# Kernel optimization log

Measured on AMD Instinct MI355X. Metric: run time of the kernel, lower is better.

## Reference

```python
import jax, jax.numpy as jnp
import numpy as np


def _gcn_layer(ann, adj, Wa, ba, W2, b2):
    # ann: [B,N,F], adj: [B,E,N,N], Wa: [E,F,U], ba: [E,U], W2: [F,U], b2: [U]
    # per-edge-type linear, fused as one batched einsum -> [B,E,N,U]
    h = jnp.einsum('bnf,efu->benu', ann, Wa) + ba[None, :, None, :]
    # adjacency matmul per edge type: [B,E,N,N] @ [B,E,N,U]
    h = jnp.einsum('benm,bemu->benu', adj, h)
    # sum over edge types + residual linear + activation (tanh)
    out = h.sum(axis=1) + jnp.einsum('bnf,fu->bnu', ann, W2) + b2
    return jnp.tanh(out)


def setup_inputs() -> dict:
    key = jax.random.key(0)
    ks = jax.random.split(key, 10)
    B, N, F, E, U = 32, 1024, 32, 4, 32
    s = 1.0 / np.sqrt(F)
    s1 = 1.0 / np.sqrt(F + U)
    return {
        'n_tensor': jax.random.normal(ks[0], (B, N, F), dtype=jnp.float32),
        'adj_tensor': jax.random.uniform(ks[1], (B, E, N, N), dtype=jnp.float32),
        'W_adj0': jax.random.normal(ks[2], (E, F, U), dtype=jnp.float32) * s,
        'b_adj0': jax.random.normal(ks[3], (E, U), dtype=jnp.float32) * s,
        'W2_0': jax.random.normal(ks[4], (F, U), dtype=jnp.float32) * s,
        'b2_0': jax.random.normal(ks[5], (U,), dtype=jnp.float32) * s,
        'W_adj1': jax.random.normal(ks[6], (E, F + U, U), dtype=jnp.float32) * s1,
        'b_adj1': jax.random.normal(ks[7], (E, U), dtype=jnp.float32) * s1,
        'W2_1': jax.random.normal(ks[8], (F + U, U), dtype=jnp.float32) * s1,
        'b2_1': jax.random.normal(ks[9], (U,), dtype=jnp.float32) * s1,
    }


def reference(n_tensor, adj_tensor, W_adj0, b_adj0, W2_0, b2_0,
              W_adj1, b_adj1, W2_1, b2_1):
    # layer 0: h_tensor is None -> annotations = n_tensor
    h = _gcn_layer(n_tensor, adj_tensor, W_adj0, b_adj0, W2_0, b2_0)
    # layer 1: annotations = cat(n_tensor, hidden)
    ann1 = jnp.concatenate([n_tensor, h], axis=-1)
    h = _gcn_layer(ann1, adj_tensor, W_adj1, b_adj1, W2_1, b2_1)
    return h
```

## Files before the change

kernel.cpp:

```cpp
#include <hip/hip_runtime.h>
#include <math.h>

#define Bb 32
#define Nn 1024
#define Ee 4
#define Uu 32

template <int F, int FA>
__global__ __launch_bounds__(256) void pre_kernel(
    const float* __restrict__ annA, const float* __restrict__ annB,
    const float* __restrict__ Wa, const float* __restrict__ ba,
    const float* __restrict__ W2, const float* __restrict__ b2,
    float* __restrict__ hpre_t, float* __restrict__ res)
{
    const int e = blockIdx.y;
    __shared__ float wlds[F * Uu];
    __shared__ float blds[Uu];
    const int tid = threadIdx.x;
    const float* wsrc = (e < 4) ? (Wa + (size_t)e * F * Uu) : W2;
    const float* bsrc = (e < 4) ? (ba + (size_t)e * Uu) : b2;
    for (int i = tid; i < F * Uu; i += 256) wlds[i] = wsrc[i];
    if (tid < Uu) blds[tid] = bsrc[tid];
    __syncthreads();

    const int g = blockIdx.x * 256 + tid;
    const int b = g >> 10;
    const int n = g & 1023;

    float4 a4[F / 4];
    {
        const float4* rA = (const float4*)(annA + (size_t)g * FA);
#pragma unroll
        for (int i = 0; i < FA / 4; ++i) a4[i] = rA[i];
        if constexpr (F > FA) {
            const float4* rB = (const float4*)(annB + (size_t)g * (F - FA));
#pragma unroll
            for (int i = 0; i < (F - FA) / 4; ++i) a4[FA / 4 + i] = rB[i];
        }
    }

    float4 acc[8];
    const float4* bb = (const float4*)blds;
#pragma unroll
    for (int uq = 0; uq < 8; ++uq) acc[uq] = bb[uq];
    const float4* w4 = (const float4*)wlds;
#pragma unroll
    for (int f4 = 0; f4 < F / 4; ++f4) {
        const float4 av = a4[f4];
#pragma unroll
        for (int c = 0; c < 4; ++c) {
            const float s = (c == 0) ? av.x : (c == 1) ? av.y : (c == 2) ? av.z : av.w;
#pragma unroll
            for (int uq = 0; uq < 8; ++uq) {
                const float4 w = w4[(f4 * 4 + c) * 8 + uq];
                acc[uq].x = fmaf(s, w.x, acc[uq].x);
                acc[uq].y = fmaf(s, w.y, acc[uq].y);
                acc[uq].z = fmaf(s, w.z, acc[uq].z);
                acc[uq].w = fmaf(s, w.w, acc[uq].w);
            }
        }
    }
    if (e < 4) {
        float* dst = hpre_t + ((size_t)(b * 4 + e) * Uu) * Nn + n;
#pragma unroll
        for (int uq = 0; uq < 8; ++uq) {
            dst[(uq * 4 + 0) * Nn] = acc[uq].x;
            dst[(uq * 4 + 1) * Nn] = acc[uq].y;
            dst[(uq * 4 + 2) * Nn] = acc[uq].z;
            dst[(uq * 4 + 3) * Nn] = acc[uq].w;
        }
    } else {
        float4* dst = (float4*)(res + (size_t)g * Uu);
#pragma unroll
        for (int uq = 0; uq < 8; ++uq) dst[uq] = acc[uq];
    }
}

__global__ __launch_bounds__(256) void gcn_main_kernel(
    const float* __restrict__ adj,
    const float* __restrict__ hpre_t,
    const float* __restrict__ res,
    float* __restrict__ out)
{
    __shared__ float hbuf[2][Uu * 64];

    const int bid = blockIdx.x;
    const int swz = (bid & 7) * 128 + (bid >> 3);
    const int b = swz >> 5;
    const int n0 = (swz & 31) * 32;
    const int tid = threadIdx.x;
    const int w = tid >> 6;
    const int lane = tid & 63;
    const int gu = lane >> 4;
    const int ms = lane & 15;
    const int wrow = n0 + w * 8;

    float acc[8][8];
#pragma unroll
    for (int r = 0; r < 8; ++r)
#pragma unroll
        for (int j = 0; j < 8; ++j) acc[r][j] = 0.f;

    const float* adjb = adj + (size_t)b * Ee * Nn * Nn;
    const float* hpb = hpre_t + (size_t)b * Ee * Uu * Nn;

    const int fi0 = tid, fi1 = tid + 256;
    const int su0 = fi0 >> 4, sm0 = fi0 & 15;
    const int su1 = fi1 >> 4, sm1 = fi1 & 15;

    float4 adjA[8], adjB[8];
    float4 h0, h1;

    {
        const float* ap = adjb + (size_t)wrow * Nn + ms * 4;
#pragma unroll
        for (int r = 0; r < 8; ++r) adjA[r] = *(const float4*)(ap + (size_t)r * Nn);
        h0 = *(const float4*)(hpb + (size_t)su0 * Nn + sm0 * 4);
        h1 = *(const float4*)(hpb + (size_t)su1 * Nn + sm1 * 4);
    }

#define GCN_BODY(CUR, ALT, T)                                                   \
    {                                                                           \
        const int t_ = (T);                                                     \
        float* hb = hbuf[t_ & 1];                                               \
        ((float4*)hb)[fi0] = h0;                  \
        ((float4*)hb)[fi1] = h1;                                                \
        const int tn_ = (t_ < 63) ? t_ + 1 : 63;                                \
        const int e2_ = tn_ >> 4, c2_ = tn_ & 15;                               \
        const float* ap_ = adjb + ((size_t)e2_ * Nn + wrow) * Nn + c2_ * 64 + ms * 4; \
        _Pragma("unroll")                                                       \
        for (int r = 0; r < 8; ++r) ALT[r] = *(const float4*)(ap_ + (size_t)r * Nn); \
        const float* hc_ = hpb + (size_t)e2_ * Uu * Nn + c2_ * 64;              \
        h0 = *(const float4*)(hc_ + (size_t)su0 * Nn + sm0 * 4);                \
        h1 = *(const float4*)(hc_ + (size_t)su1 * Nn + sm1 * 4);                \
        asm volatile("s_waitcnt lgkmcnt(0)" ::: "memory");                      \
        __builtin_amdgcn_s_barrier();                                           \
        __builtin_amdgcn_sched_barrier(0);                                      \
        _Pragma("unroll")                                                       \
        for (int j = 0; j < 8; ++j) {                                           \
            const float4 hv = *(const float4*)(hb + (gu * 8 + j) * 64 + ms * 4); \
            _Pragma("unroll")                                                   \
            for (int r = 0; r < 8; ++r) {                                       \
                float t = fmaf(CUR[r].x, hv.x, acc[r][j]);                      \
                t = fmaf(CUR[r].y, hv.y, t);                                    \
                t = fmaf(CUR[r].z, hv.z, t);                                    \
                acc[r][j] = fmaf(CUR[r].w, hv.w, t);                            \
            }                                                                   \
        }                                                                       \
    }

    for (int t = 0; t < 64; t += 2) {
        GCN_BODY(adjA, adjB, t);
        GCN_BODY(adjB, adjA, t + 1);
    }
#undef GCN_BODY

#pragma unroll
    for (int r = 0; r < 8; ++r)
#pragma unroll
        for (int j = 0; j < 8; ++j) {
            float v = acc[r][j];
            v += __shfl_xor(v, 1);
            v += __shfl_xor(v, 2);
            v += __shfl_xor(v, 4);
            v += __shfl_xor(v, 8);
            acc[r][j] = v;
        }

#pragma unroll
    for (int r = 0; r < 8; ++r) {
        if (ms == r) {
            const int n = wrow + r;
            const float* rp = res + ((size_t)b * Nn + n) * Uu + gu * 8;
            float* op = out + ((size_t)b * Nn + n) * Uu + gu * 8;
            const float4 r0 = *(const float4*)(rp);
            const float4 r1 = *(const float4*)(rp + 4);
            float4 o0, o1;
            o0.x = tanhf(acc[r][0] + r0.x);
            o0.y = tanhf(acc[r][1] + r0.y);
            o0.z = tanhf(acc[r][2] + r0.z);
            o0.w = tanhf(acc[r][3] + r0.w);
            o1.x = tanhf(acc[r][4] + r1.x);
            o1.y = tanhf(acc[r][5] + r1.y);
            o1.z = tanhf(acc[r][6] + r1.z);
            o1.w = tanhf(acc[r][7] + r1.w);
            *(float4*)(op) = o0;
            *(float4*)(op + 4) = o1;
        }
    }
}

extern "C" void kernel_launch(void* const* d_in, const int* in_sizes, int n_in,
                              void* d_out, int out_size, void* d_ws, size_t ws_size,
                              hipStream_t stream)
{
    const float* n_tensor = (const float*)d_in[0];
    const float* adj      = (const float*)d_in[1];
    const float* W_adj0   = (const float*)d_in[2];
    const float* b_adj0   = (const float*)d_in[3];
    const float* W2_0     = (const float*)d_in[4];
    const float* b2_0     = (const float*)d_in[5];
    const float* W_adj1   = (const float*)d_in[6];
    const float* b_adj1   = (const float*)d_in[7];
    const float* W2_1     = (const float*)d_in[8];
    const float* b2_1     = (const float*)d_in[9];
    float* outp = (float*)d_out;

    float* ws   = (float*)d_ws;
    float* hpre = ws;
    float* resb = ws + (size_t)4 * 1024 * 1024;
    float* h0   = ws + (size_t)5 * 1024 * 1024;

    dim3 pre_grid(128, 5);

    pre_kernel<32, 32><<<pre_grid, 256, 0, stream>>>(n_tensor, nullptr, W_adj0, b_adj0,
                                                     W2_0, b2_0, hpre, resb);
    gcn_main_kernel<<<1024, 256, 0, stream>>>(adj, hpre, resb, h0);

    pre_kernel<64, 32><<<pre_grid, 256, 0, stream>>>(n_tensor, h0, W_adj1, b_adj1,
                                                     W2_1, b2_1, hpre, resb);
    gcn_main_kernel<<<1024, 256, 0, stream>>>(adj, hpre, resb, outp);
}
```

Before: 426.9 us.

## Triple-buffer GCN main loop with direct global-to-LDS loads and smaller row tiles

Rewrites the adjacency-matmul main loop as a three-stage pipeline. The hidden-feature tiles are loaded straight into LDS with global_load_lds instead of being staged through registers, and the loop waits on vmcnt before a barrier. Each block now covers 16 rows instead of 32, launched over 2048 blocks, with 4 rows per wave, which halves the accumulator and adjacency register footprint and allows more waves in flight for this memory-bound stream of adj reads. The cost is twice as many loads of the hidden tile per batch, plus reliance on hand-counted vmcnt values for correctness.

```diff
diff --git a/kernel.cpp b/kernel.cpp
--- a/kernel.cpp
+++ b/kernel.cpp
@@ -1,7 +1,6 @@
 #include <hip/hip_runtime.h>
 #include <math.h>
 
-#define Bb 32
 #define Nn 1024
 #define Ee 4
 #define Uu 32
@@ -82,81 +81,90 @@
     const float* __restrict__ res,
     float* __restrict__ out)
 {
-    __shared__ float hbuf[2][Uu * 64];
+    __shared__ float hbuf[3][Uu * 64];
 
     const int bid = blockIdx.x;
-    const int swz = (bid & 7) * 128 + (bid >> 3);
-    const int b = swz >> 5;
-    const int n0 = (swz & 31) * 32;
+    const int swz = (bid & 7) * 256 + (bid >> 3);
+    const int b = swz >> 6;
+    const int n0 = (swz & 63) * 16;
     const int tid = threadIdx.x;
     const int w = tid >> 6;
     const int lane = tid & 63;
     const int gu = lane >> 4;
     const int ms = lane & 15;
-    const int wrow = n0 + w * 8;
-
-    float acc[8][8];
-#pragma unroll
-    for (int r = 0; r < 8; ++r)
+    const int wrow = n0 + w * 4;
+
+    const float* adjb = adj + (size_t)b * Ee * Nn * Nn;
+    const float* hpb  = hpre_t + (size_t)b * Ee * Uu * Nn;
+    const int l4 = lane >> 4, l15 = lane & 15;
+
+    float acc[4][8];
+#pragma unroll
+    for (int r = 0; r < 4; ++r)
 #pragma unroll
         for (int j = 0; j < 8; ++j) acc[r][j] = 0.f;
 
-    const float* adjb = adj + (size_t)b * Ee * Nn * Nn;
-    const float* hpb = hpre_t + (size_t)b * Ee * Uu * Nn;
-
-    const int fi0 = tid, fi1 = tid + 256;
-    const int su0 = fi0 >> 4, sm0 = fi0 & 15;
-    const int su1 = fi1 >> 4, sm1 = fi1 & 15;
-
-    float4 adjA[8], adjB[8];
-    float4 h0, h1;
-
-    {
-        const float* ap = adjb + (size_t)wrow * Nn + ms * 4;
-#pragma unroll
-        for (int r = 0; r < 8; ++r) adjA[r] = *(const float4*)(ap + (size_t)r * Nn);
-        h0 = *(const float4*)(hpb + (size_t)su0 * Nn + sm0 * 4);
-        h1 = *(const float4*)(hpb + (size_t)su1 * Nn + sm1 * 4);
-    }
-
-#define GCN_BODY(CUR, ALT, T)                                                   \
+    float4 av0[4], av1[4], av2[4];
+
+#define ISSUE(AV, PH, T)                                                        \
     {                                                                           \
-        const int t_ = (T);                                                     \
-        float* hb = hbuf[t_ & 1];                                               \
-        ((float4*)hb)[fi0] = h0;                  \
-        ((float4*)hb)[fi1] = h1;                                                \
-        const int tn_ = (t_ < 63) ? t_ + 1 : 63;                                \
-        const int e2_ = tn_ >> 4, c2_ = tn_ & 15;                               \
-        const float* ap_ = adjb + ((size_t)e2_ * Nn + wrow) * Nn + c2_ * 64 + ms * 4; \
+        const int e_ = (T) >> 4, c_ = (T) & 15;                                 \
+        const float* ap_ = adjb + ((size_t)(e_ * Nn + wrow)) * Nn + c_ * 64 + ms * 4; \
+        AV[0] = *(const float4*)(ap_);                                          \
+        AV[1] = *(const float4*)(ap_ + Nn);                                     \
+        AV[2] = *(const float4*)(ap_ + 2 * Nn);                                 \
+        AV[3] = *(const float4*)(ap_ + 3 * Nn);                                 \
+        const float* hs_ = hpb + (size_t)e_ * Uu * Nn + c_ * 64 + l15 * 4;      \
+        __builtin_amdgcn_global_load_lds(                                       \
+            (const __attribute__((address_space(1))) void*)(hs_ + (size_t)(8 * w + l4) * Nn),     \
+            (__attribute__((address_space(3))) void*)(&hbuf[PH][(8 * w) * 64]), 16, 0, 0);        \
+        __builtin_amdgcn_global_load_lds(                                       \
+            (const __attribute__((address_space(1))) void*)(hs_ + (size_t)(8 * w + 4 + l4) * Nn), \
+            (__attribute__((address_space(3))) void*)(&hbuf[PH][(8 * w + 4) * 64]), 16, 0, 0);    \
+    }
+
+#define COMPUTE(AV, PH)                                                         \
+    {                                                                           \
         _Pragma("unroll")                                                       \
-        for (int r = 0; r < 8; ++r) ALT[r] = *(const float4*)(ap_ + (size_t)r * Nn); \
-        const float* hc_ = hpb + (size_t)e2_ * Uu * Nn + c2_ * 64;              \
-        h0 = *(const float4*)(hc_ + (size_t)su0 * Nn + sm0 * 4);                \
-        h1 = *(const float4*)(hc_ + (size_t)su1 * Nn + sm1 * 4);                \
-        asm volatile("s_waitcnt lgkmcnt(0)" ::: "memory");                      \
+        for (int j = 0; j < 8; ++j) {                                           \
+            const float4 hv = *(const float4*)(&hbuf[PH][(gu * 8 + j) * 64 + ms * 4]); \
+            _Pragma("unroll")                                                   \
+            for (int r = 0; r < 4; ++r) {                                       \
+                float t0 = fmaf(AV[r].x, hv.x, acc[r][j]);                      \
+                t0 = fmaf(AV[r].y, hv.y, t0);                                   \
+                t0 = fmaf(AV[r].z, hv.z, t0);                                   \
+                acc[r][j] = fmaf(AV[r].w, hv.w, t0);                            \
+            }                                                                   \
+        }                                                                       \
+    }
+
+#define WAITBAR(N)                                                              \
+    {                                                                           \
+        __builtin_amdgcn_sched_barrier(0);                                      \
+        asm volatile("s_waitcnt vmcnt(" #N ")" ::: "memory");                   \
         __builtin_amdgcn_s_barrier();                                           \
         __builtin_amdgcn_sched_barrier(0);                                      \
-        _Pragma("unroll")                                                       \
-        for (int j = 0; j < 8; ++j) {                                           \
-            const float4 hv = *(const float4*)(hb + (gu * 8 + j) * 64 + ms * 4); \
-            _Pragma("unroll")                                                   \
-            for (int r = 0; r < 8; ++r) {                                       \
-                float t = fmaf(CUR[r].x, hv.x, acc[r][j]);                      \
-                t = fmaf(CUR[r].y, hv.y, t);                                    \
-                t = fmaf(CUR[r].z, hv.z, t);                                    \
-                acc[r][j] = fmaf(CUR[r].w, hv.w, t);                            \
-            }                                                                   \
-        }                                                                       \
-    }
-
-    for (int t = 0; t < 64; t += 2) {
-        GCN_BODY(adjA, adjB, t);
-        GCN_BODY(adjB, adjA, t + 1);
-    }
-#undef GCN_BODY
-
-#pragma unroll
-    for (int r = 0; r < 8; ++r)
+    }
+
+    ISSUE(av0, 0, 0);
+    ISSUE(av1, 1, 1);
+
+    for (int t = 0; t < 60; t += 3) {
+        WAITBAR(6); ISSUE(av2, 2, t + 2); COMPUTE(av0, 0);
+        WAITBAR(6); ISSUE(av0, 0, t + 3); COMPUTE(av1, 1);
+        WAITBAR(6); ISSUE(av1, 1, t + 4); COMPUTE(av2, 2);
+    }
+    WAITBAR(6); ISSUE(av2, 2, 62); COMPUTE(av0, 0);
+    WAITBAR(6); ISSUE(av0, 0, 63); COMPUTE(av1, 1);
+    WAITBAR(6); COMPUTE(av2, 2);
+    WAITBAR(0); COMPUTE(av0, 0);
+
+#undef ISSUE
+#undef COMPUTE
+#undef WAITBAR
+
+#pragma unroll
+    for (int r = 0; r < 4; ++r)
 #pragma unroll
         for (int j = 0; j < 8; ++j) {
             float v = acc[r][j];
@@ -168,7 +176,7 @@
         }
 
 #pragma unroll
-    for (int r = 0; r < 8; ++r) {
+    for (int r = 0; r < 4; ++r) {
         if (ms == r) {
             const int n = wrow + r;
             const float* rp = res + ((size_t)b * Nn + n) * Uu + gu * 8;
@@ -215,9 +223,9 @@
 
     pre_kernel<32, 32><<<pre_grid, 256, 0, stream>>>(n_tensor, nullptr, W_adj0, b_adj0,
                                                      W2_0, b2_0, hpre, resb);
-    gcn_main_kernel<<<1024, 256, 0, stream>>>(adj, hpre, resb, h0);
+    gcn_main_kernel<<<2048, 256, 0, stream>>>(adj, hpre, resb, h0);
 
     pre_kernel<64, 32><<<pre_grid, 256, 0, stream>>>(n_tensor, h0, W_adj1, b_adj1,
                                                      W2_1, b2_1, hpre, resb);
-    gcn_main_kernel<<<1024, 256, 0, stream>>>(adj, hpre, resb, outp);
+    gcn_main_kernel<<<2048, 256, 0, stream>>>(adj, hpre, resb, outp);
 }
```

Result: slower. 647.4 us (+51.6%).

## Split-K gcn main kernel across waves with direct h loads and LDS reduction

Applied to the files above, without the earlier changes.

Each block now covers 8 rows instead of 32, and the four waves split the m dimension (256 columns each) instead of splitting rows. Each wave loads the h tile directly from global memory into registers, which removes the LDS staging, the per-step barriers and the double-buffer pipeline. Partial sums from the four waves are combined through shared memory before the tanh epilogue. The grid grows fourfold for more parallelism, but h is now reloaded per wave from global/L2 and there is no explicit prefetch, so latency hiding depends on occupancy (launch_bounds 256,2).

```diff
diff --git a/kernel.cpp b/kernel.cpp
--- a/kernel.cpp
+++ b/kernel.cpp
@@ -1,7 +1,6 @@
 #include <hip/hip_runtime.h>
 #include <math.h>
 
-#define Bb 32
 #define Nn 1024
 #define Ee 4
 #define Uu 32
@@ -76,24 +75,27 @@
     }
 }
 
-__global__ __launch_bounds__(256) void gcn_main_kernel(
+__global__ __launch_bounds__(256, 2) void gcn_main_kernel(
     const float* __restrict__ adj,
     const float* __restrict__ hpre_t,
     const float* __restrict__ res,
     float* __restrict__ out)
 {
-    __shared__ float hbuf[2][Uu * 64];
+    __shared__ float part[4][8][Uu];
 
     const int bid = blockIdx.x;
-    const int swz = (bid & 7) * 128 + (bid >> 3);
-    const int b = swz >> 5;
-    const int n0 = (swz & 31) * 32;
+    const int swz = (bid & 7) * 512 + (bid >> 3);
+    const int b = swz >> 7;
+    const int n0 = (swz & 127) * 8;
     const int tid = threadIdx.x;
     const int w = tid >> 6;
     const int lane = tid & 63;
     const int gu = lane >> 4;
     const int ms = lane & 15;
-    const int wrow = n0 + w * 8;
+
+    const float* adjb = adj + (size_t)b * Ee * Nn * Nn;
+    const float* hpb  = hpre_t + (size_t)b * Ee * Uu * Nn;
+    const int mbase = w * 256 + ms * 4;
 
     float acc[8][8];
 #pragma unroll
@@ -101,59 +103,26 @@
 #pragma unroll
         for (int j = 0; j < 8; ++j) acc[r][j] = 0.f;
 
-    const float* adjb = adj + (size_t)b * Ee * Nn * Nn;
-    const float* hpb = hpre_t + (size_t)b * Ee * Uu * Nn;
-
-    const int fi0 = tid, fi1 = tid + 256;
-    const int su0 = fi0 >> 4, sm0 = fi0 & 15;
-    const int su1 = fi1 >> 4, sm1 = fi1 & 15;
-
-    float4 adjA[8], adjB[8];
-    float4 h0, h1;
-
-    {
-        const float* ap = adjb + (size_t)wrow * Nn + ms * 4;
+#pragma unroll 2
+    for (int it = 0; it < 16; ++it) {
+        const int e = it >> 2, sub = it & 3;
+        const float* ap = adjb + ((size_t)e * Nn + n0) * Nn + mbase + sub * 64;
+        const float* hp = hpb + ((size_t)e * Uu + gu * 8) * Nn + mbase + sub * 64;
+        float4 av[8], hv[8];
 #pragma unroll
-        for (int r = 0; r < 8; ++r) adjA[r] = *(const float4*)(ap + (size_t)r * Nn);
-        h0 = *(const float4*)(hpb + (size_t)su0 * Nn + sm0 * 4);
-        h1 = *(const float4*)(hpb + (size_t)su1 * Nn + sm1 * 4);
+        for (int r = 0; r < 8; ++r) av[r] = *(const float4*)(ap + (size_t)r * Nn);
+#pragma unroll
+        for (int j = 0; j < 8; ++j) hv[j] = *(const float4*)(hp + (size_t)j * Nn);
+#pragma unroll
+        for (int j = 0; j < 8; ++j)
+#pragma unroll
+            for (int r = 0; r < 8; ++r) {
+                float t0 = fmaf(av[r].x, hv[j].x, acc[r][j]);
+                t0 = fmaf(av[r].y, hv[j].y, t0);
+                t0 = fmaf(av[r].z, hv[j].z, t0);
+                acc[r][j] = fmaf(av[r].w, hv[j].w, t0);
+            }
     }
-
-#define GCN_BODY(CUR, ALT, T)                                                   \
-    {                                                                           \
-        const int t_ = (T);                                                     \
-        float* hb = hbuf[t_ & 1];                                               \
-        ((float4*)hb)[fi0] = h0;                  \
-        ((float4*)hb)[fi1] = h1;                                                \
-        const int tn_ = (t_ < 63) ? t_ + 1 : 63;                                \
-        const int e2_ = tn_ >> 4, c2_ = tn_ & 15;                               \
-        const float* ap_ = adjb + ((size_t)e2_ * Nn + wrow) * Nn + c2_ * 64 + ms * 4; \
-        _Pragma("unroll")                                                       \
-        for (int r = 0; r < 8; ++r) ALT[r] = *(const float4*)(ap_ + (size_t)r * Nn); \
-        const float* hc_ = hpb + (size_t)e2_ * Uu * Nn + c2_ * 64;              \
-        h0 = *(const float4*)(hc_ + (size_t)su0 * Nn + sm0 * 4);                \
-        h1 = *(const float4*)(hc_ + (size_t)su1 * Nn + sm1 * 4);                \
-        asm volatile("s_waitcnt lgkmcnt(0)" ::: "memory");                      \
-        __builtin_amdgcn_s_barrier();                                           \
-        __builtin_amdgcn_sched_barrier(0);                                      \
-        _Pragma("unroll")                                                       \
-        for (int j = 0; j < 8; ++j) {                                           \
-            const float4 hv = *(const float4*)(hb + (gu * 8 + j) * 64 + ms * 4); \
-            _Pragma("unroll")                                                   \
-            for (int r = 0; r < 8; ++r) {                                       \
-                float t = fmaf(CUR[r].x, hv.x, acc[r][j]);                      \
-                t = fmaf(CUR[r].y, hv.y, t);                                    \
-                t = fmaf(CUR[r].z, hv.z, t);                                    \
-                acc[r][j] = fmaf(CUR[r].w, hv.w, t);                            \
-            }                                                                   \
-        }                                                                       \
-    }
-
-    for (int t = 0; t < 64; t += 2) {
-        GCN_BODY(adjA, adjB, t);
-        GCN_BODY(adjB, adjA, t + 1);
-    }
-#undef GCN_BODY
 
 #pragma unroll
     for (int r = 0; r < 8; ++r)
@@ -170,23 +139,17 @@
 #pragma unroll
     for (int r = 0; r < 8; ++r) {
         if (ms == r) {
-            const int n = wrow + r;
-            const float* rp = res + ((size_t)b * Nn + n) * Uu + gu * 8;
-            float* op = out + ((size_t)b * Nn + n) * Uu + gu * 8;
-            const float4 r0 = *(const float4*)(rp);
-            const float4 r1 = *(const float4*)(rp + 4);
-            float4 o0, o1;
-            o0.x = tanhf(acc[r][0] + r0.x);
-            o0.y = tanhf(acc[r][1] + r0.y);
-            o0.z = tanhf(acc[r][2] + r0.z);
-            o0.w = tanhf(acc[r][3] + r0.w);
-            o1.x = tanhf(acc[r][4] + r1.x);
-            o1.y = tanhf(acc[r][5] + r1.y);
-            o1.z = tanhf(acc[r][6] + r1.z);
-            o1.w = tanhf(acc[r][7] + r1.w);
-            *(float4*)(op) = o0;
-            *(float4*)(op + 4) = o1;
+#pragma unroll
+            for (int j = 0; j < 8; ++j) part[w][r][gu * 8 + j] = acc[r][j];
         }
+    }
+    __syncthreads();
+
+    {
+        const int r = tid >> 5, u = tid & 31;
+        const float v = part[0][r][u] + part[1][r][u] + part[2][r][u] + part[3][r][u];
+        const size_t oi = ((size_t)b * Nn + n0 + r) * Uu + u;
+        out[oi] = tanhf(v + res[oi]);
     }
 }
 
@@ -215,9 +178,9 @@
 
     pre_kernel<32, 32><<<pre_grid, 256, 0, stream>>>(n_tensor, nullptr, W_adj0, b_adj0,
                                                      W2_0, b2_0, hpre, resb);
-    gcn_main_kernel<<<1024, 256, 0, stream>>>(adj, hpre, resb, h0);
+    gcn_main_kernel<<<4096, 256, 0, stream>>>(adj, hpre, resb, h0);
 
     pre_kernel<64, 32><<<pre_grid, 256, 0, stream>>>(n_tensor, h0, W_adj1, b_adj1,
                                                      W2_1, b2_1, hpre, resb);
-    gcn_main_kernel<<<1024, 256, 0, stream>>>(adj, hpre, resb, outp);
+    gcn_main_kernel<<<4096, 256, 0, stream>>>(adj, hpre, resb, outp);
 }
```

Result: slower. 518.8 us (+21.5%).
